# Performance work log

Hardware: AMD Instinct MI355X
Metric: run time of the kernel (lower is better)

## Reference

```python
import jax, jax.numpy as jnp
import numpy as np

N = 8192        # number of nodes (adjacency is N x N)
F_IN = 256      # in_features
F_OUT = 256     # out_features


def setup_inputs() -> dict:
    key = jax.random.key(0)
    k_x, k_adj, k_kernel, k_bias, k_beta = jax.random.split(key, 5)
    x = jax.random.normal(k_x, (N, F_IN), dtype=jnp.float32)
    adj = jax.random.uniform(k_adj, (N, N), dtype=jnp.float32)  # dense non-negative adjacency buffer
    # xavier-uniform-like scale for the kernel
    limit = float(np.sqrt(6.0 / (F_IN + F_OUT)))
    kernel = jax.random.uniform(k_kernel, (F_IN, F_OUT), dtype=jnp.float32, minval=-limit, maxval=limit)
    bias = 0.01 * jax.random.normal(k_bias, (F_OUT,), dtype=jnp.float32)
    beta = 0.01 * jax.random.normal(k_beta, (N,), dtype=jnp.float32)
    return {"x": x, "adj": adj, "kernel": kernel, "bias": bias, "beta": beta}


def reference(x, adj, kernel, bias, beta):
    # Original: diag(1/(rowsum(adj)+beta)) @ (adj + diag(beta)) @ x @ kernel + bias
    # Fused form: row-scale and diagonal-add applied without materializing NxN diag matrices.
    scale = jnp.reciprocal(jnp.sum(adj, axis=1) + beta)          # [N]
    agg = adj @ x + beta[:, None] * x                             # (adj + diag(beta)) @ x  -> [N, F_IN]
    return (scale[:, None] * agg) @ kernel + bias                 # [N, F_OUT]
```

## Files before the change

kernel.cpp:

```cpp
#include <hip/hip_runtime.h>
#include <hip/hip_bf16.h>


typedef __attribute__((ext_vector_type(8))) short  short8;
typedef __attribute__((ext_vector_type(4))) short  bf16x4;
typedef __attribute__((ext_vector_type(4))) float  floatx4;

#define N_NODES 8192
#define F_DIM   256
#define BK      64
#define NSTEPS  (N_NODES / BK)

#define ASYNC16(g, l)                                                          \
  __builtin_amdgcn_global_load_lds(                                           \
      (const __attribute__((address_space(1))) void*)(g),                     \
      (__attribute__((address_space(3))) void*)(l), 16, 0, 0)

__device__ __forceinline__ unsigned short f2bf(float f) {
  unsigned u = __float_as_uint(f);
  return (unsigned short)((u + 0x7FFFu + ((u >> 16) & 1u)) >> 16);
}

__device__ __forceinline__ short8 pack_bf16x8(floatx4 a, floatx4 b) {
  short8 r;
  r[0] = (short)f2bf(a.x);
  r[1] = (short)f2bf(a.y);
  r[2] = (short)f2bf(a.z);
  r[3] = (short)f2bf(a.w);
  r[4] = (short)f2bf(b.x);
  r[5] = (short)f2bf(b.y);
  r[6] = (short)f2bf(b.z);
  r[7] = (short)f2bf(b.w);
  return r;
}

__global__ __launch_bounds__(256) void tile_bf16_kernel(
    const float* __restrict__ src, unsigned short* __restrict__ dst, int K) {
  const int Nn = F_DIM;
  int cid = blockIdx.x * 256 + threadIdx.x;
  int per_kblk = Nn * 4;
  int kblk = cid / per_kblk;
  int rem  = cid - kblk * per_kblk;
  int n16 = rem >> 6;
  int kg  = (rem >> 4) & 3;
  int nl  = rem & 15;
  int n = n16 * 16 + nl;
  int k = kblk * 32 + kg * 8;
  const float* s = src + (size_t)k * Nn + n;
  floatx4 v0, v1;
  v0.x = s[0];
  v0.y = s[(size_t)Nn];
  v0.z = s[(size_t)2 * Nn];
  v0.w = s[(size_t)3 * Nn];
  v1.x = s[(size_t)4 * Nn];
  v1.y = s[(size_t)5 * Nn];
  v1.z = s[(size_t)6 * Nn];
  v1.w = s[(size_t)7 * Nn];
  *(short8*)(dst + (size_t)cid * 8) = pack_bf16x8(v0, v1);
}

#define AB(i) (smem + (i) * 4096)
#define BB(i) (smem + 12288 + (i) * 32768)

#define STAGE_B(sidx, c)                                                       \
  {                                                                            \
    const unsigned short* bs_ = bsrc + (size_t)(sidx) * 16384;                 \
    char* bd_ = BB(c) + (w << 10);                                             \
    ASYNC16(bs_,          bd_);                                                \
    ASYNC16(bs_ +  4096,  bd_ +  8192);                                        \
    ASYNC16(bs_ +  8192,  bd_ + 16384);                                        \
    ASYNC16(bs_ + 12288,  bd_ + 24576);                                        \
  }

#define WRITE_A(c)                                                             \
  {                                                                            \
    rsum += (areg.x + areg.y) + (areg.z + areg.w);                             \
    bf16x4 pk_;                                                                \
    pk_[0] = (short)f2bf(areg.x);                                              \
    pk_[1] = (short)f2bf(areg.y);                                              \
    pk_[2] = (short)f2bf(areg.z);                                              \
    pk_[3] = (short)f2bf(areg.w);                                              \
    *(bf16x4*)(AB(c) + awoff) = pk_;                                           \
  }

#define MFMA16(a, b, c) __builtin_amdgcn_mfma_f32_16x16x32_bf16(a, b, c, 0, 0, 0)

#define COMPUTE(c)                                                             \
  {                                                                            \
    const char* Ab_ = AB(c);                                                   \
    const char* Bb_ = BB(c);                                                   \
    short8 a00 = *(const short8*)(Ab_ + aoff00);                               \
    short8 a01 = *(const short8*)(Ab_ + aoff01);                               \
    short8 a10 = *(const short8*)(Ab_ + aoff10);                               \
    short8 a11 = *(const short8*)(Ab_ + aoff11);                               \
    short8 b00 = *(const short8*)(Bb_ + boff00);                               \
    short8 b01 = *(const short8*)(Bb_ + boff01);                               \
    short8 b10 = *(const short8*)(Bb_ + boff10);                               \
    short8 b11 = *(const short8*)(Bb_ + boff11);                               \
    acc[0][0] = MFMA16(a00, b00, acc[0][0]);                                   \
    acc[1][0] = MFMA16(a01, b00, acc[1][0]);                                   \
    acc[0][1] = MFMA16(a00, b01, acc[0][1]);                                   \
    acc[1][1] = MFMA16(a01, b01, acc[1][1]);                                   \
    acc[0][0] = MFMA16(a10, b10, acc[0][0]);                                   \
    acc[1][0] = MFMA16(a11, b10, acc[1][0]);                                   \
    acc[0][1] = MFMA16(a10, b11, acc[0][1]);                                   \
    acc[1][1] = MFMA16(a11, b11, acc[1][1]);                                   \
  }

#define FULL_ITER(sidx, c)                                                     \
  asm volatile("s_waitcnt vmcnt(4)" ::: "memory");                             \
  WRITE_A((c + 1) % 3);                                                        \
  areg = *(const floatx4*)(asrc + (size_t)((sidx) + 2) * BK);                  \
  asm volatile("s_waitcnt lgkmcnt(0)" ::: "memory");                           \
  asm volatile("s_barrier" ::: "memory");                                      \
  STAGE_B((sidx) + 2, (c + 2) % 3);                                           \
  COMPUTE(c);

__global__ __launch_bounds__(512, 2) void fused_kernel(
    const float* __restrict__ adj, const unsigned short* __restrict__ xbt,
    const float* __restrict__ x, const float* __restrict__ beta,
    const float* __restrict__ bias, const unsigned short* __restrict__ wbt,
    float* __restrict__ out) {
  __shared__ __attribute__((aligned(16))) char smem[110592];
  float* sscale = (float*)(smem + 49152);
  float* sbeta  = (float*)(smem + 49280);

  const int tid = threadIdx.x;
  const int w   = tid >> 6;
  const int l   = tid & 63;
  const int kq  = l >> 4;
  const int ml  = l & 15;
  const int r7  = ml & 7;
  const int m0  = blockIdx.x * 32;

  const int arow = tid >> 4;
  const int akc  = tid & 15;
  const float* asrc = adj + (size_t)(m0 + arow) * N_NODES + akc * 4;
  const int awoff = arow * 128 + ((((akc >> 1) ^ (arow & 7))) << 4) + (akc & 1) * 8;
  const unsigned short* bsrc = xbt + (size_t)tid * 8;

  const int aoff00 = (0 * 16 + ml) * 128 + (((0 * 4 + kq) ^ r7) << 4);
  const int aoff01 = (1 * 16 + ml) * 128 + (((0 * 4 + kq) ^ r7) << 4);
  const int aoff10 = (0 * 16 + ml) * 128 + (((1 * 4 + kq) ^ r7) << 4);
  const int aoff11 = (1 * 16 + ml) * 128 + (((1 * 4 + kq) ^ r7) << 4);
  const int boff00 = 0 * 16384 + (w * 2 + 0) * 1024 + kq * 256 + ml * 16;
  const int boff01 = 0 * 16384 + (w * 2 + 1) * 1024 + kq * 256 + ml * 16;
  const int boff10 = 1 * 16384 + (w * 2 + 0) * 1024 + kq * 256 + ml * 16;
  const int boff11 = 1 * 16384 + (w * 2 + 1) * 1024 + kq * 256 + ml * 16;

  floatx4 acc[2][2];
  const floatx4 zf4 = {0.f, 0.f, 0.f, 0.f};
  acc[0][0] = zf4; acc[0][1] = zf4; acc[1][0] = zf4; acc[1][1] = zf4;
  float rsum = 0.f;
  floatx4 areg;

  areg = *(const floatx4*)(asrc);
  STAGE_B(0, 0);
  asm volatile("s_waitcnt vmcnt(4)" ::: "memory");
  WRITE_A(0);
  areg = *(const floatx4*)(asrc + BK);
  STAGE_B(1, 1);
  asm volatile("s_waitcnt vmcnt(4)" ::: "memory");
  WRITE_A(1);
  areg = *(const floatx4*)(asrc + 2 * BK);
  asm volatile("s_waitcnt lgkmcnt(0)" ::: "memory");
  asm volatile("s_barrier" ::: "memory");
  STAGE_B(2, 2);
  COMPUTE(0);

  for (int t = 0; t < 41; ++t) {
    const int s0 = 3 * t + 1;
    FULL_ITER(s0,     1);
    FULL_ITER(s0 + 1, 2);
    FULL_ITER(s0 + 2, 0);
  }
  FULL_ITER(124, 1);
  FULL_ITER(125, 2);
  asm volatile("s_waitcnt vmcnt(4)" ::: "memory");
  WRITE_A(1);
  asm volatile("s_waitcnt lgkmcnt(0)" ::: "memory");
  asm volatile("s_barrier" ::: "memory");
  COMPUTE(0);
  asm volatile("s_waitcnt vmcnt(0)" ::: "memory");
  asm volatile("s_barrier" ::: "memory");
  COMPUTE(1);

  __syncthreads();

  {
    const float* xs = x + (size_t)m0 * F_DIM + tid * 4;
    char* xd = smem + 16384 + (w << 10);
#pragma unroll
    for (int q = 0; q < 4; ++q) ASYNC16(xs + q * 2048, xd + q * 8192);
  }
  {
    float rs = rsum;
    rs += __shfl_xor(rs, 1);
    rs += __shfl_xor(rs, 2);
    rs += __shfl_xor(rs, 4);
    rs += __shfl_xor(rs, 8);
    if ((l & 15) == 0) {
      int row = w * 4 + (l >> 4);
      float b = beta[m0 + row];
      sbeta[row]  = b;
      sscale[row] = 1.0f / (rs + b);
    }
  }
  __syncthreads();

  const float* xl = (const float*)(smem + 16384);
  unsigned short* G = (unsigned short*)smem;
#pragma unroll
  for (int nf = 0; nf < 2; ++nf) {
    int col = w * 32 + nf * 16 + ml;
    int chunk = col >> 3;
#pragma unroll
    for (int mf = 0; mf < 2; ++mf)
#pragma unroll
      for (int r = 0; r < 4; ++r) {
        int row = mf * 16 + kq * 4 + r;
        float g = sscale[row] * (acc[mf][nf][r] + sbeta[row] * xl[row * F_DIM + col]);
        int slot = (chunk & 24) | ((chunk ^ row) & 7);
        G[row * 256 + slot * 8 + (col & 7)] = f2bf(g);
      }
  }
  __syncthreads();

  floatx4 acc2[2][2];
  acc2[0][0] = zf4; acc2[0][1] = zf4; acc2[1][0] = zf4; acc2[1][1] = zf4;
#pragma unroll
  for (int s2 = 0; s2 < 8; ++s2) {
    int c = s2 * 4 + kq;
    int sl = (c & 24) | ((c ^ ml) & 7);
    short8 ag0 = *(const short8*)(G + (ml)      * 256 + sl * 8);
    short8 ag1 = *(const short8*)(G + (16 + ml) * 256 + sl * 8);
    const unsigned short* wb = wbt + s2 * 8192 + (w * 2) * 512 + kq * 128 + ml * 8;
    short8 wv0 = *(const short8*)(wb);
    short8 wv1 = *(const short8*)(wb + 512);
    acc2[0][0] = MFMA16(ag0, wv0, acc2[0][0]);
    acc2[1][0] = MFMA16(ag1, wv0, acc2[1][0]);
    acc2[0][1] = MFMA16(ag0, wv1, acc2[0][1]);
    acc2[1][1] = MFMA16(ag1, wv1, acc2[1][1]);
  }
#pragma unroll
  for (int nf = 0; nf < 2; ++nf) {
    int col = w * 32 + nf * 16 + ml;
    float bv = bias[col];
#pragma unroll
    for (int mf = 0; mf < 2; ++mf)
#pragma unroll
      for (int r = 0; r < 4; ++r) {
        int row = m0 + mf * 16 + kq * 4 + r;
        out[(size_t)row * F_DIM + col] = acc2[mf][nf][r] + bv;
      }
  }
}

extern "C" void kernel_launch(void* const* d_in, const int* in_sizes, int n_in,
                              void* d_out, int out_size, void* d_ws, size_t ws_size,
                              hipStream_t stream) {
  const float* x    = (const float*)d_in[0];
  const float* adj  = (const float*)d_in[1];
  const float* kern = (const float*)d_in[2];
  const float* bias = (const float*)d_in[3];
  const float* beta = (const float*)d_in[4];
  float* out = (float*)d_out;

  char* ws = (char*)d_ws;
  unsigned short* xbt = (unsigned short*)ws;
  unsigned short* wbt = xbt + (size_t)N_NODES * F_DIM;

  tile_bf16_kernel<<<(N_NODES * F_DIM / 8) / 256, 256, 0, stream>>>(x, xbt, N_NODES);
  tile_bf16_kernel<<<(F_DIM * F_DIM / 8) / 256, 256, 0, stream>>>(kern, wbt, F_DIM);
  fused_kernel<<<256, 512, 0, stream>>>(adj, xbt, x, beta, bias, wbt, out);
}
```

Baseline: 440.2 us.

## Load x operand fragments directly into registers instead of staging through LDS

Each wave's B operand (the bf16 pre-packed x tiles) is now read straight from global memory into registers with double buffering, instead of being copied asynchronously into a triple-buffered LDS region. This cuts shared memory from about 108KB to 48KB, removes LDS read traffic for B, and simplifies the pipeline to one barrier per step. In exchange, B loads are exposed to global latency without an explicit vmcnt wait, the A-operand swizzle and fragment ordering are reshuffled, and register pressure rises.

Result: faster. 428.5 us (-2.6%).

```diff
diff --git a/kernel.cpp b/kernel.cpp
--- a/kernel.cpp
+++ b/kernel.cpp
@@ -59,69 +59,62 @@
   *(short8*)(dst + (size_t)cid * 8) = pack_bf16x8(v0, v1);
 }
 
-#define AB(i) (smem + (i) * 4096)
-#define BB(i) (smem + 12288 + (i) * 32768)
-
-#define STAGE_B(sidx, c)                                                       \
+#define MFMA16(a, b, c) __builtin_amdgcn_mfma_f32_16x16x32_bf16(a, b, c, 0, 0, 0)
+#define AB(c) (smem + (c) * 4096)
+
+#define LOADB(dst, sv)                                                         \
+  _Pragma("unroll") for (int kb_ = 0; kb_ < 2; ++kb_)                          \
+  _Pragma("unroll") for (int nf_ = 0; nf_ < 2; ++nf_)                          \
+      dst[kb_][nf_] = *(const short8*)(bgl + (size_t)(sv) * 16384 +            \
+                                       kb_ * 8192 + nf_ * 512);
+
+#define COPYB()                                                                \
+  _Pragma("unroll") for (int kb_ = 0; kb_ < 2; ++kb_)                          \
+  _Pragma("unroll") for (int nf_ = 0; nf_ < 2; ++nf_) bc[kb_][nf_] = bn[kb_][nf_];
+
+#define WRITE_A(cw)                                                            \
   {                                                                            \
-    const unsigned short* bs_ = bsrc + (size_t)(sidx) * 16384;                 \
-    char* bd_ = BB(c) + (w << 10);                                             \
-    ASYNC16(bs_,          bd_);                                                \
-    ASYNC16(bs_ +  4096,  bd_ +  8192);                                        \
-    ASYNC16(bs_ +  8192,  bd_ + 16384);                                        \
-    ASYNC16(bs_ + 12288,  bd_ + 24576);                                        \
-  }
-
-#define WRITE_A(c)                                                             \
-  {                                                                            \
-    rsum += (areg.x + areg.y) + (areg.z + areg.w);                             \
+    rsum += (areg_w.x + areg_w.y) + (areg_w.z + areg_w.w);                     \
     bf16x4 pk_;                                                                \
-    pk_[0] = (short)f2bf(areg.x);                                              \
-    pk_[1] = (short)f2bf(areg.y);                                              \
-    pk_[2] = (short)f2bf(areg.z);                                              \
-    pk_[3] = (short)f2bf(areg.w);                                              \
-    *(bf16x4*)(AB(c) + awoff) = pk_;                                           \
-  }
-
-#define MFMA16(a, b, c) __builtin_amdgcn_mfma_f32_16x16x32_bf16(a, b, c, 0, 0, 0)
+    pk_[0] = (short)f2bf(areg_w.x);                                            \
+    pk_[1] = (short)f2bf(areg_w.y);                                            \
+    pk_[2] = (short)f2bf(areg_w.z);                                            \
+    pk_[3] = (short)f2bf(areg_w.w);                                            \
+    *(bf16x4*)(AB(cw) + awoff) = pk_;                                          \
+  }
 
 #define COMPUTE(c)                                                             \
   {                                                                            \
     const char* Ab_ = AB(c);                                                   \
-    const char* Bb_ = BB(c);                                                   \
-    short8 a00 = *(const short8*)(Ab_ + aoff00);                               \
-    short8 a01 = *(const short8*)(Ab_ + aoff01);                               \
-    short8 a10 = *(const short8*)(Ab_ + aoff10);                               \
-    short8 a11 = *(const short8*)(Ab_ + aoff11);                               \
-    short8 b00 = *(const short8*)(Bb_ + boff00);                               \
-    short8 b01 = *(const short8*)(Bb_ + boff01);                               \
-    short8 b10 = *(const short8*)(Bb_ + boff10);                               \
-    short8 b11 = *(const short8*)(Bb_ + boff11);                               \
-    acc[0][0] = MFMA16(a00, b00, acc[0][0]);                                   \
-    acc[1][0] = MFMA16(a01, b00, acc[1][0]);                                   \
-    acc[0][1] = MFMA16(a00, b01, acc[0][1]);                                   \
-    acc[1][1] = MFMA16(a01, b01, acc[1][1]);                                   \
-    acc[0][0] = MFMA16(a10, b10, acc[0][0]);                                   \
-    acc[1][0] = MFMA16(a11, b10, acc[1][0]);                                   \
-    acc[0][1] = MFMA16(a10, b11, acc[0][1]);                                   \
-    acc[1][1] = MFMA16(a11, b11, acc[1][1]);                                   \
-  }
-
-#define FULL_ITER(sidx, c)                                                     \
-  asm volatile("s_waitcnt vmcnt(4)" ::: "memory");                             \
-  WRITE_A((c + 1) % 3);                                                        \
-  areg = *(const floatx4*)(asrc + (size_t)((sidx) + 2) * BK);                  \
-  asm volatile("s_waitcnt lgkmcnt(0)" ::: "memory");                           \
-  asm volatile("s_barrier" ::: "memory");                                      \
-  STAGE_B((sidx) + 2, (c + 2) % 3);                                           \
-  COMPUTE(c);
+    short8 a00 = *(const short8*)(Ab_ + aoff00);                \
+    short8 a01 = *(const short8*)(Ab_ + aoff01);                \
+    short8 a10 = *(const short8*)(Ab_ + aoff10);                \
+    short8 a11 = *(const short8*)(Ab_ + aoff11);                \
+    acc[0][0] = MFMA16(a00, bc[0][0], acc[0][0]);                              \
+    acc[0][1] = MFMA16(a00, bc[0][1], acc[0][1]);                              \
+    acc[1][0] = MFMA16(a10, bc[0][0], acc[1][0]);                              \
+    acc[1][1] = MFMA16(a10, bc[0][1], acc[1][1]);                              \
+    acc[0][0] = MFMA16(a01, bc[1][0], acc[0][0]);                              \
+    acc[0][1] = MFMA16(a01, bc[1][1], acc[0][1]);                              \
+    acc[1][0] = MFMA16(a11, bc[1][0], acc[1][0]);                              \
+    acc[1][1] = MFMA16(a11, bc[1][1], acc[1][1]);                              \
+  }
+
+#define FULL_ITER(sv, c, cw)                                                   \
+  LOADB(bn, (sv) + 1);                                                         \
+  areg_l = *(const floatx4*)(agl + (size_t)((sv) + 2) * BK);                   \
+  asm volatile("s_waitcnt lgkmcnt(0)\n\ts_barrier" ::: "memory");              \
+  WRITE_A(cw);                                                                 \
+  COMPUTE(c);                                                                  \
+  COPYB();                                                                     \
+  areg_w = areg_l;
 
 __global__ __launch_bounds__(512, 2) void fused_kernel(
     const float* __restrict__ adj, const unsigned short* __restrict__ xbt,
     const float* __restrict__ x, const float* __restrict__ beta,
     const float* __restrict__ bias, const unsigned short* __restrict__ wbt,
     float* __restrict__ out) {
-  __shared__ __attribute__((aligned(16))) char smem[110592];
+  __shared__ __attribute__((aligned(16))) char smem[49408];
   float* sscale = (float*)(smem + 49152);
   float* sbeta  = (float*)(smem + 49280);
 
@@ -130,59 +123,52 @@
   const int l   = tid & 63;
   const int kq  = l >> 4;
   const int ml  = l & 15;
-  const int r7  = ml & 7;
   const int m0  = blockIdx.x * 32;
 
   const int arow = tid >> 4;
-  const int akc  = tid & 15;
-  const float* asrc = adj + (size_t)(m0 + arow) * N_NODES + akc * 4;
-  const int awoff = arow * 128 + ((((akc >> 1) ^ (arow & 7))) << 4) + (akc & 1) * 8;
-  const unsigned short* bsrc = xbt + (size_t)tid * 8;
-
-  const int aoff00 = (0 * 16 + ml) * 128 + (((0 * 4 + kq) ^ r7) << 4);
-  const int aoff01 = (1 * 16 + ml) * 128 + (((0 * 4 + kq) ^ r7) << 4);
-  const int aoff10 = (0 * 16 + ml) * 128 + (((1 * 4 + kq) ^ r7) << 4);
-  const int aoff11 = (1 * 16 + ml) * 128 + (((1 * 4 + kq) ^ r7) << 4);
-  const int boff00 = 0 * 16384 + (w * 2 + 0) * 1024 + kq * 256 + ml * 16;
-  const int boff01 = 0 * 16384 + (w * 2 + 1) * 1024 + kq * 256 + ml * 16;
-  const int boff10 = 1 * 16384 + (w * 2 + 0) * 1024 + kq * 256 + ml * 16;
-  const int boff11 = 1 * 16384 + (w * 2 + 1) * 1024 + kq * 256 + ml * 16;
+  const int ag4  = tid & 15;
+  const float* agl = adj + (size_t)(m0 + arow) * N_NODES + ag4 * 4;
+  const int awoff = arow * 128 + (((ag4 >> 1) ^ (arow & 7)) << 4) + (ag4 & 1) * 8;
+
+  const int aoff00 = (0 * 16 + ml) * 128 + (((0 * 4 + kq) ^ (ml & 7)) << 4);
+  const int aoff01 = (0 * 16 + ml) * 128 + (((1 * 4 + kq) ^ (ml & 7)) << 4);
+  const int aoff10 = (1 * 16 + ml) * 128 + (((0 * 4 + kq) ^ (ml & 7)) << 4);
+  const int aoff11 = (1 * 16 + ml) * 128 + (((1 * 4 + kq) ^ (ml & 7)) << 4);
+
+  const unsigned short* bgl = xbt + w * 1024 + kq * 128 + ml * 8;
 
   floatx4 acc[2][2];
   const floatx4 zf4 = {0.f, 0.f, 0.f, 0.f};
   acc[0][0] = zf4; acc[0][1] = zf4; acc[1][0] = zf4; acc[1][1] = zf4;
   float rsum = 0.f;
-  floatx4 areg;
-
-  areg = *(const floatx4*)(asrc);
-  STAGE_B(0, 0);
-  asm volatile("s_waitcnt vmcnt(4)" ::: "memory");
-  WRITE_A(0);
-  areg = *(const floatx4*)(asrc + BK);
-  STAGE_B(1, 1);
-  asm volatile("s_waitcnt vmcnt(4)" ::: "memory");
+  floatx4 areg_w, areg_l;
+  short8 bc[2][2], bn[2][2];
+
+  {
+    floatx4 a0v = *(const floatx4*)(agl);
+    LOADB(bc, 0);
+    areg_w = *(const floatx4*)(agl + BK);
+    rsum += (a0v.x + a0v.y) + (a0v.z + a0v.w);
+    bf16x4 pk;
+    pk[0] = (short)f2bf(a0v.x);
+    pk[1] = (short)f2bf(a0v.y);
+    pk[2] = (short)f2bf(a0v.z);
+    pk[3] = (short)f2bf(a0v.w);
+    *(bf16x4*)(AB(0) + awoff) = pk;
+  }
+
+  for (int t = 0; t < 42; ++t) {
+    const int s0 = 3 * t;
+    FULL_ITER(s0,     0, 1);
+    FULL_ITER(s0 + 1, 1, 2);
+    FULL_ITER(s0 + 2, 2, 0);
+  }
+  LOADB(bn, 127);
+  asm volatile("s_waitcnt lgkmcnt(0)\n\ts_barrier" ::: "memory");
   WRITE_A(1);
-  areg = *(const floatx4*)(asrc + 2 * BK);
-  asm volatile("s_waitcnt lgkmcnt(0)" ::: "memory");
-  asm volatile("s_barrier" ::: "memory");
-  STAGE_B(2, 2);
   COMPUTE(0);
-
-  for (int t = 0; t < 41; ++t) {
-    const int s0 = 3 * t + 1;
-    FULL_ITER(s0,     1);
-    FULL_ITER(s0 + 1, 2);
-    FULL_ITER(s0 + 2, 0);
-  }
-  FULL_ITER(124, 1);
-  FULL_ITER(125, 2);
-  asm volatile("s_waitcnt vmcnt(4)" ::: "memory");
-  WRITE_A(1);
-  asm volatile("s_waitcnt lgkmcnt(0)" ::: "memory");
-  asm volatile("s_barrier" ::: "memory");
-  COMPUTE(0);
-  asm volatile("s_waitcnt vmcnt(0)" ::: "memory");
-  asm volatile("s_barrier" ::: "memory");
+  COPYB();
+  asm volatile("s_waitcnt lgkmcnt(0)\n\ts_barrier" ::: "memory");
   COMPUTE(1);
 
   __syncthreads();
```
